# Kernel tuning notes

Measured on AMD Instinct MI355X. Metric: run time of the kernel, lower is better.

Reference implementation:

```python
import jax, jax.numpy as jnp
import numpy as np

C, CB, W, N = 256, 64, 32, 16
F = CB * W  # 2048 lstm features


def setup_inputs() -> dict:
    key = jax.random.key(0)
    ks = jax.random.split(key, 8)
    sc = 1.0 / np.sqrt(F)  # matches torch LSTM uniform(-1/sqrt(H), 1/sqrt(H)) scale
    return {
        "latent": jax.random.normal(ks[0], (N, C, W, W), jnp.float32),
        "w_in": jax.random.normal(ks[1], (CB, C), jnp.float32) * 0.05,
        "b_in": jnp.zeros((CB,), jnp.float32),
        "w_ih0": jax.random.normal(ks[2], (4 * F, F), jnp.float32) * sc,
        "w_hh0": jax.random.normal(ks[3], (4 * F, F), jnp.float32) * sc,
        "b_ih0": jnp.zeros((4 * F,), jnp.float32),
        "b_hh0": jnp.zeros((4 * F,), jnp.float32),
        "w_ih1": jax.random.normal(ks[4], (4 * F, F), jnp.float32) * sc,
        "w_hh1": jax.random.normal(ks[5], (4 * F, F), jnp.float32) * sc,
        "b_ih1": jnp.zeros((4 * F,), jnp.float32),
        "b_hh1": jnp.zeros((4 * F,), jnp.float32),
        "w_out": jax.random.normal(ks[6], (C, CB), jnp.float32) * 0.05,
        "b_out": jnp.zeros((C,), jnp.float32),
    }


def _lstm_cell(xt, h, c, w_ih, w_hh, b):
    # torch gate order: i, f, g, o
    g = xt @ w_ih.T + h @ w_hh.T + b
    i, f, gg, o = jnp.split(g, 4, axis=-1)
    c = jax.nn.sigmoid(f) * c + jax.nn.sigmoid(i) * jnp.tanh(gg)
    h = jax.nn.sigmoid(o) * jnp.tanh(c)
    return h, c


def reference(latent, w_in, b_in, w_ih0, w_hh0, b_ih0, b_hh0,
              w_ih1, w_hh1, b_ih1, b_hh1, w_out, b_out):
    n, ch, w, hgt = latent.shape
    # bottleneck_in: 1x1 conv (Normalizer.NONE / Activation.NONE -> identity)
    x = jnp.einsum('nchw,oc->nohw', latent, w_in) + b_in[None, :, None, None]  # (N,CB,W,H)
    # (N,CB,W,H) -> (N,W,H,CB) -> (N,W,H*CB) -> (W,N,F)
    seq = x.transpose(0, 2, 3, 1).reshape(n, w, -1).transpose(1, 0, 2)

    b0 = b_ih0 + b_hh0
    b1 = b_ih1 + b_hh1

    def step2(carry, xt):
        h0, c0, h1, c1 = carry
        h0, c0 = _lstm_cell(xt, h0, c0, w_ih0, w_hh0, b0)
        h1, c1 = _lstm_cell(h0, h1, c1, w_ih1, w_hh1, b1)
        return (h0, c0, h1, c1), h1

    z = jnp.zeros((n, seq.shape[-1]), latent.dtype)
    state, outs = jax.lax.scan(step2, (z, z, z, z), seq)
    last = outs[-1]  # out[-1] of full-sequence pass

    def ar_step(carry, _):
        st, xt = carry
        st, y = step2(st, xt)
        return (st, y), y

    _, ar_outs = jax.lax.scan(ar_step, (state, last), None, length=w - 1)
    seq_out = jnp.concatenate([last[None], ar_outs], axis=0)  # (W,N,F)

    # (W,N,F) -> (N,W,F) -> (N,W,H,CB) -> (N,CB,W,H)
    gen = seq_out.transpose(1, 0, 2).reshape(n, w, hgt, -1).transpose(0, 3, 1, 2)
    gen = jnp.einsum('nchw,oc->nohw', gen, w_out) + b_out[None, :, None, None]
    # stitch along spatial W axis (dim=2)
    return jnp.concatenate([latent, gen], axis=2)
```

## Files before the change

### kernel.cpp

```cpp
#include <hip/hip_runtime.h>
#include <hip/hip_bf16.h>

#define NB   16
#define FDIM 2048
#define GDIM 8192
#define WSEQ 32
#define CDIM 256
#define CBD  64
#define HGT  32

#define AGENTSC __HIP_MEMORY_SCOPE_AGENT

typedef float f32x4 __attribute__((ext_vector_type(4)));
typedef long  l64x2 __attribute__((ext_vector_type(2)));
typedef _Float16 f16x4 __attribute__((ext_vector_type(4)));
typedef unsigned char u8;

__device__ __forceinline__ float sigf(float x) { return 1.f / (1.f + __expf(-x)); }

__device__ __forceinline__ u8 f32_to_fp8(float f) {
    int w = __builtin_amdgcn_cvt_pk_fp8_f32(f, f, 0, 0);
    return (u8)(w & 0xff);
}

__global__ __launch_bounds__(256) void pack_w(
        const float* __restrict__ wih0, const float* __restrict__ whh0,
        const float* __restrict__ wih1, const float* __restrict__ whh1,
        u8* __restrict__ W0, u8* __restrict__ W1) {
    __shared__ u8 FW[16][4112];
    int b = blockIdx.x;
    int mat = b >> 9, tile = b & 511;
    const float* wih = mat ? wih1 : wih0;
    const float* whh = mat ? whh1 : whh0;
    int p = tile & 1, jt = tile >> 1;
    int tid = threadIdx.x;
    for (int it = 0; it < 32; it += 4) {
        float4 f[4][2];
#pragma unroll
        for (int r = 0; r < 4; ++r) {
            int c = (it + r) & 15, srcsel = (it + r) >> 4;
            int gate = p * 2 + (c >> 3);
            int rr = gate * FDIM + jt * 8 + (c & 7);
            const float* s = (srcsel ? whh : wih) + (size_t)rr * FDIM + tid * 8;
            f[r][0] = *(const float4*)(s);
            f[r][1] = *(const float4*)(s + 4);
        }
#pragma unroll
        for (int r = 0; r < 4; ++r) {
            int c = (it + r) & 15, srcsel = (it + r) >> 4;
            int w0 = __builtin_amdgcn_cvt_pk_fp8_f32(f[r][0].x, f[r][0].y, 0, 0);
            w0     = __builtin_amdgcn_cvt_pk_fp8_f32(f[r][0].z, f[r][0].w, w0, 1);
            int w1 = __builtin_amdgcn_cvt_pk_fp8_f32(f[r][1].x, f[r][1].y, 0, 0);
            w1     = __builtin_amdgcn_cvt_pk_fp8_f32(f[r][1].z, f[r][1].w, w1, 1);
            *(int2*)&FW[c][srcsel * 2048 + tid * 8] = make_int2(w0, w1);
        }
    }
    __syncthreads();
    u8* base = (mat ? W1 : W0) + (size_t)tile * 65536;
#pragma unroll
    for (int w = 0; w < 16; ++w) {
        int q = w * 256 + tid;
        int kc2 = q >> 6, lane = q & 63;
        int c = lane & 15, kg = lane >> 4;
        l64x2 v;
        v.x = *(const long*)&FW[c][kc2 * 64 + kg * 8];
        v.y = *(const long*)&FW[c][kc2 * 64 + 32 + kg * 8];
        *(l64x2*)(base + (size_t)q * 16) = v;
    }
}

__global__ void bias_k(const float* __restrict__ bih0, const float* __restrict__ bhh0,
                       const float* __restrict__ bih1, const float* __restrict__ bhh1,
                       float* __restrict__ b0, float* __restrict__ b1) {
    int i = blockIdx.x * blockDim.x + threadIdx.x;
    if (i < GDIM)            b0[i] = bih0[i] + bhh0[i];
    else if (i < 2 * GDIM) { int j = i - GDIM; b1[j] = bih1[j] + bhh1[j]; }
}

__global__ __launch_bounds__(256) void conv_in(const float* __restrict__ latent,
                        const float* __restrict__ w_in, const float* __restrict__ b_in,
                        u8* __restrict__ seqbP) {
    __shared__ float lat[CDIM * HGT];
    __shared__ float hv[FDIM];
    int b = blockIdx.x; int n = b >> 5; int t = b & 31;
    int tid = threadIdx.x;
    for (int i = 0; i < 32; ++i) {
        int flat = i * 256 + tid;
        int c = flat >> 5, h = flat & 31;
        lat[flat] = latent[(((size_t)n * CDIM + c) * WSEQ + t) * HGT + h];
    }
    __syncthreads();
    int cb = tid & 63;
    int hb = tid >> 6;
    float acc[8];
#pragma unroll
    for (int k = 0; k < 8; ++k) acc[k] = b_in[cb];
    for (int c = 0; c < CDIM; ++c) {
        float wv = w_in[cb * CDIM + c];
#pragma unroll
        for (int k = 0; k < 8; ++k) acc[k] += lat[c * HGT + (hb + k * 4)] * wv;
    }
#pragma unroll
    for (int k = 0; k < 8; ++k) hv[k * 256 + tid] = acc[k];
    __syncthreads();
    union { u8 by[8]; long l; } pk;
#pragma unroll
    for (int i = 0; i < 8; ++i) pk.by[i] = f32_to_fp8(hv[tid * 8 + i]);
    *(long*)(seqbP + (size_t)t * 32768 + (tid >> 2) * 512 + (tid & 3) * 128 + n * 8) = pk.l;
}

__device__ __forceinline__ void load8_plain(const u8* p, long* f) {
    asm volatile("global_load_dwordx2 %0, %1, off"             : "=v"(f[0]) : "v"(p));
    asm volatile("global_load_dwordx2 %0, %1, off offset:512"  : "=v"(f[1]) : "v"(p));
    asm volatile("global_load_dwordx2 %0, %1, off offset:1024" : "=v"(f[2]) : "v"(p));
    asm volatile("global_load_dwordx2 %0, %1, off offset:1536" : "=v"(f[3]) : "v"(p));
    asm volatile("global_load_dwordx2 %0, %1, off offset:2048" : "=v"(f[4]) : "v"(p));
    asm volatile("global_load_dwordx2 %0, %1, off offset:2560" : "=v"(f[5]) : "v"(p));
    asm volatile("global_load_dwordx2 %0, %1, off offset:3072" : "=v"(f[6]) : "v"(p));
    asm volatile("global_load_dwordx2 %0, %1, off offset:3584" : "=v"(f[7]) : "v"(p));
}

__device__ __forceinline__ void vm_wait0() {
    asm volatile("s_waitcnt vmcnt(0)" ::: "memory");
    __builtin_amdgcn_sched_barrier(0);
}

__device__ __forceinline__ void sync_lds() {
    asm volatile("s_waitcnt lgkmcnt(0)" ::: "memory");
    __builtin_amdgcn_s_barrier();
    asm volatile("" ::: "memory");
}

__device__ __forceinline__ f32x4 mfma8(long a, long b, f32x4 acc) {
    return __builtin_amdgcn_mfma_f32_16x16x32_fp8_fp8(a, b, acc, 0, 0, 0);
}

__device__ __forceinline__ void mma8_reg(const long* f, const l64x2* b, f32x4& acc) {
#pragma unroll
    for (int i = 0; i < 4; ++i) {
        acc = mfma8(f[2 * i],     b[i].x, acc);
        acc = mfma8(f[2 * i + 1], b[i].y, acc);
    }
}
__device__ __forceinline__ void mma8_lds(const long* f, const l64x2* bb, f32x4& acc) {
#pragma unroll
    for (int i = 0; i < 4; ++i) {
        l64x2 bl = bb[(size_t)i * 64];
        acc = mfma8(f[2 * i],     bl.x, acc);
        acc = mfma8(f[2 * i + 1], bl.y, acc);
    }
}

__device__ __forceinline__ void store_frag(_Float16* part16, int t, int w,
                                           int kg, int la, f32x4 acc) {
    f16x4 h;
#pragma unroll
    for (int q = 0; q < 4; ++q) h[q] = (_Float16)acc[q];
    *(f16x4*)&part16[(((t * 16 + w) * 16) + la) * 20 + kg * 4] = h;
}

__device__ __forceinline__ void cell_tail16(const _Float16* part16, int jt, int tid,
        float bi, float bf, float bg, float bo, float& cr,
        u8* oA, u8* oB, float* seqSlot) {
    if (tid < 128) {
        int m = tid >> 3, jj = tid & 7;
        float gi = 0.f, gf = 0.f, gg = 0.f, go = 0.f;
#pragma unroll
        for (int w2 = 0; w2 < 16; ++w2) {
            int i0 = (w2 * 16 + jj) * 20 + m;
            gi += (float)part16[i0];
            gf += (float)part16[i0 + 160];
            gg += (float)part16[i0 + 5120];
            go += (float)part16[i0 + 5280];
        }
        float cn = sigf(gf + bf) * cr + sigf(gi + bi) * tanhf(gg + bg);
        float h  = sigf(go + bo) * tanhf(cn);
        cr = cn;
        u8 hb = f32_to_fp8(h);
        int pos = (jt >> 2) * 512 + (jt & 3) * 128 + tid;
        __hip_atomic_store(oA + pos, hb, __ATOMIC_RELAXED, AGENTSC);
        __hip_atomic_store(oB + pos, hb, __ATOMIC_RELAXED, AGENTSC);
        if (seqSlot)
            __hip_atomic_store(seqSlot + m * FDIM + jt * 8 + jj, h,
                               __ATOMIC_RELAXED, AGENTSC);
    }
}

__device__ __forceinline__ void grid_bar(unsigned* slots) {
    __syncthreads();
    if (threadIdx.x < 64) {
        if (threadIdx.x == 0) {
            unsigned one = 1u;
            const unsigned* p = slots + blockIdx.x;
            asm volatile("global_store_dword %0, %1, off sc1"
                         :: "v"(p), "v"(one) : "memory");
        }
        const uint4* q = (const uint4*)slots + threadIdx.x;
        int guard = 0;
        while (++guard < (1 << 22)) {
            uint4 v;
            asm volatile("global_load_dwordx4 %0, %1, off sc1"
                         : "=v"(v) : "v"(q) : "memory");
            asm volatile("s_waitcnt vmcnt(0)" ::: "memory");
            if (__all((v.x & v.y & v.z & v.w) != 0u)) break;
            __builtin_amdgcn_s_sleep(1);
        }
    }
    __syncthreads();
}

__global__ __launch_bounds__(1024, 4) void recurrence(
        const u8* __restrict__ W0, const u8* __restrict__ W1,
        const u8* __restrict__ seqbP,
        const float* __restrict__ b0, const float* __restrict__ b1,
        u8* __restrict__ h0A, u8* __restrict__ h0B,
        u8* __restrict__ h1A, u8* __restrict__ h1B,
        const u8* __restrict__ zb,
        float* __restrict__ sqo, unsigned* __restrict__ arr) {
    __shared__ uint4 w1lds[8192];
    __shared__ _Float16 part16[2 * 16 * 16 * 20];
    const int jt = blockIdx.x, tid = threadIdx.x;
    const int w = tid >> 6, l = tid & 63;
    const int la = l & 15, kg = l >> 4;
    {
        const uint4* src = (const uint4*)(W1 + (size_t)jt * 131072);
        for (int i = tid; i < 8192; i += 1024) w1lds[i] = src[i];
    }
    l64x2 b0pin[8];
#pragma unroll
    for (int t = 0; t < 2; ++t)
#pragma unroll
        for (int i = 0; i < 4; ++i)
            b0pin[t * 4 + i] = *(const l64x2*)(W0 +
                ((size_t)((jt * 2 + t) * 64 + w * 4 + i) * 64 + l) * 16);
    float cr0 = 0.f, cr1 = 0.f;
    float bi0 = 0, bf0 = 0, bg0 = 0, bo0 = 0, bi1 = 0, bf1 = 0, bg1 = 0, bo1 = 0;
    if (tid < 128) {
        int j = jt * 8 + (tid & 7);
        bi0 = b0[j]; bf0 = b0[FDIM + j]; bg0 = b0[2 * FDIM + j]; bo0 = b0[3 * FDIM + j];
        bi1 = b1[j]; bf1 = b1[FDIM + j]; bg1 = b1[2 * FDIM + j]; bo1 = b1[3 * FDIM + j];
    }
    __syncthreads();

    unsigned* bs = arr;
    const l64x2* bbA = (const l64x2*)w1lds + ((size_t)(w * 4) * 64 + l);
    const l64x2* bbB = bbA + (size_t)64 * 64;
    const f32x4 z = {0.f, 0.f, 0.f, 0.f};
    const size_t wl = (size_t)w * 4096 + (size_t)l * 8;
    const size_t wh = (size_t)(w - 8) * 4096 + (size_t)l * 8;
#define HB(arrp, s) ((arrp) + (size_t)(s) * 32768)

    auto l0_phase = [&](const u8* xp, const u8* hp, u8* oA, u8* oB) {
        long f[8];
        load8_plain((w < 8) ? xp + wl : hp + wh, f);
        vm_wait0();
        f32x4 t0 = z, t1 = z;
        mma8_reg(f, b0pin, t0); mma8_reg(f, b0pin + 4, t1);
        store_frag(part16, 0, w, kg, la, t0);
        store_frag(part16, 1, w, kg, la, t1);
        sync_lds();
        cell_tail16(part16, jt, tid, bi0, bf0, bg0, bo0, cr0, oA, oB, nullptr);
    };
    auto l1_phase = [&](const u8* p1, const u8* p2, u8* oA, u8* oB, float* slot) {
        long f[8];
        load8_plain((w < 8) ? p1 + wl : p2 + wh, f);
        vm_wait0();
        f32x4 t0 = z, t1 = z;
        mma8_lds(f, bbA, t0); mma8_lds(f, bbB, t1);
        store_frag(part16, 0, w, kg, la, t0);
        store_frag(part16, 1, w, kg, la, t1);
        sync_lds();
        cell_tail16(part16, jt, tid, bi1, bf1, bg1, bo1, cr1, oA, oB, slot);
    };

    l0_phase(seqbP, zb, HB(h0A, 0), HB(h0B, 0));
    grid_bar(bs); bs += 256;

    for (int s = 0; s <= 30; ++s) {
        long f0[8], f1[8];
        const u8* a0src = (w < 8) ? seqbP + (size_t)(s + 1) * 32768 + wl
                                  : HB(h0A, s) + wh;
        const u8* a1src = (w < 8) ? HB(h0B, s) + wl
                                  : (s == 0 ? zb + wh : HB(h1A, s - 1) + wh);
        load8_plain(a0src, f0);
        load8_plain(a1src, f1);
        vm_wait0();
        f32x4 q00 = z, q01 = z, q10 = z, q11 = z;
        mma8_reg(f0, b0pin, q00); mma8_reg(f0, b0pin + 4, q01);
        mma8_lds(f1, bbA, q10);   mma8_lds(f1, bbB, q11);
        store_frag(part16, 0, w, kg, la, q00);
        store_frag(part16, 1, w, kg, la, q01);
        sync_lds();
        cell_tail16(part16, jt, tid, bi0, bf0, bg0, bo0, cr0,
                    HB(h0A, s + 1), HB(h0B, s + 1), nullptr);
        sync_lds();
        store_frag(part16, 0, w, kg, la, q10);
        store_frag(part16, 1, w, kg, la, q11);
        sync_lds();
        cell_tail16(part16, jt, tid, bi1, bf1, bg1, bo1, cr1,
                    HB(h1A, s), HB(h1B, s), nullptr);
        grid_bar(bs); bs += 256;
    }
    l1_phase(HB(h0B, 31), HB(h1A, 30), HB(h1A, 31), HB(h1B, 31), sqo);
    grid_bar(bs); bs += 256;
    for (int s = 32; s < 63; ++s) {
        l0_phase(HB(h1B, s - 1), HB(h0A, s - 1), HB(h0A, s), HB(h0B, s));
        grid_bar(bs); bs += 256;
        l1_phase(HB(h0B, s), HB(h1A, s - 1), HB(h1A, s), HB(h1B, s),
                 sqo + (size_t)(s - 31) * NB * FDIM);
        if (s != 62) { grid_bar(bs); bs += 256; }
    }
#undef HB
}

__global__ void copy_lat(const float* __restrict__ latent, float* __restrict__ out) {
    size_t i = (size_t)blockIdx.x * blockDim.x + threadIdx.x;
    if (i >= (size_t)1048576) return;
    size_t blk = i >> 8;
    size_t within = i & 255;
    float4 v = ((const float4*)latent)[i];
    ((float4*)out)[blk * 512 + within] = v;
}

__global__ __launch_bounds__(256) void gen_out(const float* __restrict__ seq_out,
                        const float* __restrict__ w_out, const float* __restrict__ b_out,
                        float* __restrict__ out) {
    __shared__ float row[32 * 65];
    int b = blockIdx.x; int n = b >> 5, t = b & 31;
    const float* src = seq_out + ((size_t)t * NB + n) * FDIM;
    for (int i = threadIdx.x; i < FDIM; i += 256)
        row[(i >> 6) * 65 + (i & 63)] = src[i];
    __syncthreads();
    for (int it = 0; it < 32; ++it) {
        int o = it * 256 + threadIdx.x;
        int c = o >> 5, h = o & 31;
        float acc = b_out[c];
#pragma unroll
        for (int cb = 0; cb < CBD; ++cb) acc += row[h * 65 + cb] * w_out[c * CBD + cb];
        out[(((size_t)n * CDIM + c) * 64 + 32 + t) * HGT + h] = acc;
    }
}

extern "C" void kernel_launch(void* const* d_in, const int* in_sizes, int n_in,
                              void* d_out, int out_size, void* d_ws, size_t ws_size,
                              hipStream_t stream) {
    const float* latent = (const float*)d_in[0];
    const float* w_in   = (const float*)d_in[1];
    const float* b_in   = (const float*)d_in[2];
    const float* w_ih0  = (const float*)d_in[3];
    const float* w_hh0  = (const float*)d_in[4];
    const float* b_ih0  = (const float*)d_in[5];
    const float* b_hh0  = (const float*)d_in[6];
    const float* w_ih1  = (const float*)d_in[7];
    const float* w_hh1  = (const float*)d_in[8];
    const float* b_ih1  = (const float*)d_in[9];
    const float* b_hh1  = (const float*)d_in[10];
    const float* w_out  = (const float*)d_in[11];
    const float* b_out  = (const float*)d_in[12];
    float* out = (float*)d_out;
    char* ws = (char*)d_ws;

    size_t off = 0;
    u8*    W0   = (u8*)(ws + off); off += (size_t)512 * 65536;
    u8*    W1   = (u8*)(ws + off); off += (size_t)512 * 65536;
    u8*    seqbP= (u8*)(ws + off); off += (size_t)WSEQ * 32768;
    float* sqo  = (float*)(ws + off); off += (size_t)WSEQ * NB * FDIM * 4;
    u8*    h0A  = (u8*)(ws + off); off += (size_t)64 * 32768;
    u8*    h0B  = (u8*)(ws + off); off += (size_t)64 * 32768;
    u8*    h1A  = (u8*)(ws + off); off += (size_t)64 * 32768;
    u8*    h1B  = (u8*)(ws + off); off += (size_t)64 * 32768;
    char*  zbase = ws + off;
    u8*    zb   = (u8*)(ws + off); off += 32768;
    unsigned* arr = (unsigned*)(ws + off); off += (size_t)94 * 1024;
    size_t zbytes = (size_t)(ws + off - zbase);
    float* b0 = (float*)(ws + off); off += (size_t)GDIM * 4;
    float* b1 = (float*)(ws + off); off += (size_t)GDIM * 4;

    if (ws_size < off) {
        hipMemsetAsync(d_out, 0, (size_t)out_size * 4, stream);
        return;
    }

    hipMemsetAsync(zbase, 0, zbytes, stream);
    pack_w<<<1024, 256, 0, stream>>>(w_ih0, w_hh0, w_ih1, w_hh1, W0, W1);
    bias_k<<<64, 256, 0, stream>>>(b_ih0, b_hh0, b_ih1, b_hh1, b0, b1);
    conv_in<<<512, 256, 0, stream>>>(latent, w_in, b_in, seqbP);
    recurrence<<<256, 1024, 0, stream>>>(W0, W1, seqbP, b0, b1,
                                         h0A, h0B, h1A, h1B, zb, sqo, arr);
    copy_lat<<<4096, 256, 0, stream>>>(latent, out);
    gen_out<<<512, 256, 0, stream>>>(sqo, w_out, b_out, out);
}
```

Before: 767.9 us.

## Pin both layers' weights in registers and run the two cell tails concurrently

Result: slower. 1.083 ms (+41.0%).

```diff
diff --git a/kernel.cpp b/kernel.cpp
--- a/kernel.cpp
+++ b/kernel.cpp
@@ -142,48 +142,37 @@
         acc = mfma8(f[2 * i + 1], b[i].y, acc);
     }
 }
-__device__ __forceinline__ void mma8_lds(const long* f, const l64x2* bb, f32x4& acc) {
-#pragma unroll
-    for (int i = 0; i < 4; ++i) {
-        l64x2 bl = bb[(size_t)i * 64];
-        acc = mfma8(f[2 * i],     bl.x, acc);
-        acc = mfma8(f[2 * i + 1], bl.y, acc);
-    }
-}
-
-__device__ __forceinline__ void store_frag(_Float16* part16, int t, int w,
+
+__device__ __forceinline__ void store_frag(_Float16* P, int t, int w,
                                            int kg, int la, f32x4 acc) {
     f16x4 h;
 #pragma unroll
     for (int q = 0; q < 4; ++q) h[q] = (_Float16)acc[q];
-    *(f16x4*)&part16[(((t * 16 + w) * 16) + la) * 20 + kg * 4] = h;
-}
-
-__device__ __forceinline__ void cell_tail16(const _Float16* part16, int jt, int tid,
+    *(f16x4*)&P[(((t * 16 + w) * 16) + la) * 20 + kg * 4] = h;
+}
+
+__device__ __forceinline__ void cell_tail16(const _Float16* P, int jt, int t2,
         float bi, float bf, float bg, float bo, float& cr,
-        u8* oA, u8* oB, float* seqSlot) {
-    if (tid < 128) {
-        int m = tid >> 3, jj = tid & 7;
-        float gi = 0.f, gf = 0.f, gg = 0.f, go = 0.f;
-#pragma unroll
-        for (int w2 = 0; w2 < 16; ++w2) {
-            int i0 = (w2 * 16 + jj) * 20 + m;
-            gi += (float)part16[i0];
-            gf += (float)part16[i0 + 160];
-            gg += (float)part16[i0 + 5120];
-            go += (float)part16[i0 + 5280];
-        }
-        float cn = sigf(gf + bf) * cr + sigf(gi + bi) * tanhf(gg + bg);
-        float h  = sigf(go + bo) * tanhf(cn);
-        cr = cn;
-        u8 hb = f32_to_fp8(h);
-        int pos = (jt >> 2) * 512 + (jt & 3) * 128 + tid;
-        __hip_atomic_store(oA + pos, hb, __ATOMIC_RELAXED, AGENTSC);
-        __hip_atomic_store(oB + pos, hb, __ATOMIC_RELAXED, AGENTSC);
-        if (seqSlot)
-            __hip_atomic_store(seqSlot + m * FDIM + jt * 8 + jj, h,
-                               __ATOMIC_RELAXED, AGENTSC);
-    }
+        u8* hOut, float* seqSlot) {
+    int m = t2 >> 3, jj = t2 & 7;
+    float gi = 0.f, gf = 0.f, gg = 0.f, go = 0.f;
+#pragma unroll
+    for (int w2 = 0; w2 < 16; ++w2) {
+        int i0 = (w2 * 16 + jj) * 20 + m;
+        gi += (float)P[i0];
+        gf += (float)P[i0 + 160];
+        gg += (float)P[i0 + 5120];
+        go += (float)P[i0 + 5280];
+    }
+    float cn = sigf(gf + bf) * cr + sigf(gi + bi) * tanhf(gg + bg);
+    float h  = sigf(go + bo) * tanhf(cn);
+    cr = cn;
+    u8 hb = f32_to_fp8(h);
+    int pos = (jt >> 2) * 512 + (jt & 3) * 128 + t2;
+    __hip_atomic_store(hOut + pos, hb, __ATOMIC_RELAXED, AGENTSC);
+    if (seqSlot)
+        __hip_atomic_store(seqSlot + m * FDIM + jt * 8 + jj, h,
+                           __ATOMIC_RELAXED, AGENTSC);
 }
 
 __device__ __forceinline__ void grid_bar(unsigned* slots) {
@@ -213,104 +202,122 @@
         const u8* __restrict__ W0, const u8* __restrict__ W1,
         const u8* __restrict__ seqbP,
         const float* __restrict__ b0, const float* __restrict__ b1,
-        u8* __restrict__ h0A, u8* __restrict__ h0B,
-        u8* __restrict__ h1A, u8* __restrict__ h1B,
+        u8* __restrict__ h0buf, u8* __restrict__ h1buf,
         const u8* __restrict__ zb,
         float* __restrict__ sqo, unsigned* __restrict__ arr) {
-    __shared__ uint4 w1lds[8192];
-    __shared__ _Float16 part16[2 * 16 * 16 * 20];
+    __shared__ _Float16 pA[2 * 16 * 16 * 20];
+    __shared__ _Float16 pB[2 * 16 * 16 * 20];
+    __shared__ u8 ldspad[49152];
     const int jt = blockIdx.x, tid = threadIdx.x;
     const int w = tid >> 6, l = tid & 63;
     const int la = l & 15, kg = l >> 4;
-    {
-        const uint4* src = (const uint4*)(W1 + (size_t)jt * 131072);
-        for (int i = tid; i < 8192; i += 1024) w1lds[i] = src[i];
-    }
-    l64x2 b0pin[8];
+    if (tid == 1023) { volatile u8* vp = ldspad; vp[0] = 1; }
+    l64x2 w0pin[8], w1pin[8];
 #pragma unroll
     for (int t = 0; t < 2; ++t)
 #pragma unroll
-        for (int i = 0; i < 4; ++i)
-            b0pin[t * 4 + i] = *(const l64x2*)(W0 +
-                ((size_t)((jt * 2 + t) * 64 + w * 4 + i) * 64 + l) * 16);
-    float cr0 = 0.f, cr1 = 0.f;
-    float bi0 = 0, bf0 = 0, bg0 = 0, bo0 = 0, bi1 = 0, bf1 = 0, bg1 = 0, bo1 = 0;
+        for (int i = 0; i < 4; ++i) {
+            size_t idx = ((size_t)((jt * 2 + t) * 64 + w * 4 + i) * 64 + l) * 16;
+            w0pin[t * 4 + i] = *(const l64x2*)(W0 + idx);
+            w1pin[t * 4 + i] = *(const l64x2*)(W1 + idx);
+        }
+    float cr = 0.f;
+    float bi = 0, bf = 0, bg = 0, bo = 0;
     if (tid < 128) {
         int j = jt * 8 + (tid & 7);
-        bi0 = b0[j]; bf0 = b0[FDIM + j]; bg0 = b0[2 * FDIM + j]; bo0 = b0[3 * FDIM + j];
-        bi1 = b1[j]; bf1 = b1[FDIM + j]; bg1 = b1[2 * FDIM + j]; bo1 = b1[3 * FDIM + j];
+        bi = b0[j]; bf = b0[FDIM + j]; bg = b0[2 * FDIM + j]; bo = b0[3 * FDIM + j];
+    } else if (tid < 256) {
+        int j = jt * 8 + (tid & 7);
+        bi = b1[j]; bf = b1[FDIM + j]; bg = b1[2 * FDIM + j]; bo = b1[3 * FDIM + j];
     }
     __syncthreads();
 
     unsigned* bs = arr;
-    const l64x2* bbA = (const l64x2*)w1lds + ((size_t)(w * 4) * 64 + l);
-    const l64x2* bbB = bbA + (size_t)64 * 64;
     const f32x4 z = {0.f, 0.f, 0.f, 0.f};
     const size_t wl = (size_t)w * 4096 + (size_t)l * 8;
     const size_t wh = (size_t)(w - 8) * 4096 + (size_t)l * 8;
-#define HB(arrp, s) ((arrp) + (size_t)(s) * 32768)
-
-    auto l0_phase = [&](const u8* xp, const u8* hp, u8* oA, u8* oB) {
-        long f[8];
-        load8_plain((w < 8) ? xp + wl : hp + wh, f);
+#define H0(s) (h0buf + (size_t)(s) * 32768)
+#define H1(s) (h1buf + (size_t)(s) * 32768)
+
+    long f0[8], f1[8];
+
+    {
+        load8_plain((w < 8) ? seqbP + wl : zb + wh, f0);
         vm_wait0();
         f32x4 t0 = z, t1 = z;
-        mma8_reg(f, b0pin, t0); mma8_reg(f, b0pin + 4, t1);
-        store_frag(part16, 0, w, kg, la, t0);
-        store_frag(part16, 1, w, kg, la, t1);
+        mma8_reg(f0, w0pin, t0); mma8_reg(f0, w0pin + 4, t1);
+        store_frag(pA, 0, w, kg, la, t0);
+        store_frag(pA, 1, w, kg, la, t1);
         sync_lds();
-        cell_tail16(part16, jt, tid, bi0, bf0, bg0, bo0, cr0, oA, oB, nullptr);
-    };
-    auto l1_phase = [&](const u8* p1, const u8* p2, u8* oA, u8* oB, float* slot) {
-        long f[8];
-        load8_plain((w < 8) ? p1 + wl : p2 + wh, f);
+        if (tid < 128)
+            cell_tail16(pA, jt, tid, bi, bf, bg, bo, cr, H0(0), nullptr);
+    }
+    for (int s = 0; s <= 30; ++s) {
+        if (w < 8) load8_plain(seqbP + (size_t)(s + 1) * 32768 + wl, f0);
+        grid_bar(bs); bs += 256;
+        if (w >= 8) {
+            load8_plain(H0(s) + wh, f0);
+            load8_plain((s ? H1(s - 1) : zb) + wh, f1);
+        } else {
+            load8_plain(H0(s) + wl, f1);
+        }
+        vm_wait0();
+        f32x4 q00 = z, q01 = z, q10 = z, q11 = z;
+        mma8_reg(f0, w0pin, q00); mma8_reg(f0, w0pin + 4, q01);
+        mma8_reg(f1, w1pin, q10); mma8_reg(f1, w1pin + 4, q11);
+        store_frag(pA, 0, w, kg, la, q00);
+        store_frag(pA, 1, w, kg, la, q01);
+        store_frag(pB, 0, w, kg, la, q10);
+        store_frag(pB, 1, w, kg, la, q11);
+        sync_lds();
+        if (tid < 128)
+            cell_tail16(pA, jt, tid, bi, bf, bg, bo, cr, H0(s + 1), nullptr);
+        else if (tid < 256)
+            cell_tail16(pB, jt, tid - 128, bi, bf, bg, bo, cr, H1(s), nullptr);
+    }
+    {
+        grid_bar(bs); bs += 256;
+        load8_plain((w < 8) ? H0(31) + wl : H1(30) + wh, f1);
         vm_wait0();
         f32x4 t0 = z, t1 = z;
-        mma8_lds(f, bbA, t0); mma8_lds(f, bbB, t1);
-        store_frag(part16, 0, w, kg, la, t0);
-        store_frag(part16, 1, w, kg, la, t1);
+        mma8_reg(f1, w1pin, t0); mma8_reg(f1, w1pin + 4, t1);
+        store_frag(pB, 0, w, kg, la, t0);
+        store_frag(pB, 1, w, kg, la, t1);
         sync_lds();
-        cell_tail16(part16, jt, tid, bi1, bf1, bg1, bo1, cr1, oA, oB, slot);
-    };
-
-    l0_phase(seqbP, zb, HB(h0A, 0), HB(h0B, 0));
-    grid_bar(bs); bs += 256;
-
-    for (int s = 0; s <= 30; ++s) {
-        long f0[8], f1[8];
-        const u8* a0src = (w < 8) ? seqbP + (size_t)(s + 1) * 32768 + wl
-                                  : HB(h0A, s) + wh;
-        const u8* a1src = (w < 8) ? HB(h0B, s) + wl
-                                  : (s == 0 ? zb + wh : HB(h1A, s - 1) + wh);
-        load8_plain(a0src, f0);
-        load8_plain(a1src, f1);
-        vm_wait0();
-        f32x4 q00 = z, q01 = z, q10 = z, q11 = z;
-        mma8_reg(f0, b0pin, q00); mma8_reg(f0, b0pin + 4, q01);
-        mma8_lds(f1, bbA, q10);   mma8_lds(f1, bbB, q11);
-        store_frag(part16, 0, w, kg, la, q00);
-        store_frag(part16, 1, w, kg, la, q01);
-        sync_lds();
-        cell_tail16(part16, jt, tid, bi0, bf0, bg0, bo0, cr0,
-                    HB(h0A, s + 1), HB(h0B, s + 1), nullptr);
-        sync_lds();
-        store_frag(part16, 0, w, kg, la, q10);
-        store_frag(part16, 1, w, kg, la, q11);
-        sync_lds();
-        cell_tail16(part16, jt, tid, bi1, bf1, bg1, bo1, cr1,
-                    HB(h1A, s), HB(h1B, s), nullptr);
+        if (tid >= 128 && tid < 256)
+            cell_tail16(pB, jt, tid - 128, bi, bf, bg, bo, cr, H1(31), sqo);
+    }
+    for (int s = 32; s < 63; ++s) {
+        if (w >= 8) load8_plain(H0(s - 1) + wh, f0);
         grid_bar(bs); bs += 256;
-    }
-    l1_phase(HB(h0B, 31), HB(h1A, 30), HB(h1A, 31), HB(h1B, 31), sqo);
-    grid_bar(bs); bs += 256;
-    for (int s = 32; s < 63; ++s) {
-        l0_phase(HB(h1B, s - 1), HB(h0A, s - 1), HB(h0A, s), HB(h0B, s));
+        if (w < 8) load8_plain(H1(s - 1) + wl, f0);
+        vm_wait0();
+        {
+            f32x4 t0 = z, t1 = z;
+            mma8_reg(f0, w0pin, t0); mma8_reg(f0, w0pin + 4, t1);
+            store_frag(pA, 0, w, kg, la, t0);
+            store_frag(pA, 1, w, kg, la, t1);
+            sync_lds();
+            if (tid < 128)
+                cell_tail16(pA, jt, tid, bi, bf, bg, bo, cr, H0(s), nullptr);
+        }
+        if (w >= 8) load8_plain(H1(s - 1) + wh, f1);
         grid_bar(bs); bs += 256;
-        l1_phase(HB(h0B, s), HB(h1A, s - 1), HB(h1A, s), HB(h1B, s),
-                 sqo + (size_t)(s - 31) * NB * FDIM);
-        if (s != 62) { grid_bar(bs); bs += 256; }
-    }
-#undef HB
+        if (w < 8) load8_plain(H0(s) + wl, f1);
+        vm_wait0();
+        {
+            f32x4 t0 = z, t1 = z;
+            mma8_reg(f1, w1pin, t0); mma8_reg(f1, w1pin + 4, t1);
+            store_frag(pB, 0, w, kg, la, t0);
+            store_frag(pB, 1, w, kg, la, t1);
+            sync_lds();
+            if (tid >= 128 && tid < 256)
+                cell_tail16(pB, jt, tid - 128, bi, bf, bg, bo, cr, H1(s),
+                            sqo + (size_t)(s - 31) * NB * FDIM);
+        }
+    }
+#undef H0
+#undef H1
 }
 
 __global__ void copy_lat(const float* __restrict__ latent, float* __restrict__ out) {
@@ -365,10 +372,8 @@
     u8*    W1   = (u8*)(ws + off); off += (size_t)512 * 65536;
     u8*    seqbP= (u8*)(ws + off); off += (size_t)WSEQ * 32768;
     float* sqo  = (float*)(ws + off); off += (size_t)WSEQ * NB * FDIM * 4;
-    u8*    h0A  = (u8*)(ws + off); off += (size_t)64 * 32768;
-    u8*    h0B  = (u8*)(ws + off); off += (size_t)64 * 32768;
-    u8*    h1A  = (u8*)(ws + off); off += (size_t)64 * 32768;
-    u8*    h1B  = (u8*)(ws + off); off += (size_t)64 * 32768;
+    u8*    h0buf= (u8*)(ws + off); off += (size_t)64 * 32768;
+    u8*    h1buf= (u8*)(ws + off); off += (size_t)64 * 32768;
     char*  zbase = ws + off;
     u8*    zb   = (u8*)(ws + off); off += 32768;
     unsigned* arr = (unsigned*)(ws + off); off += (size_t)94 * 1024;
@@ -386,7 +391,7 @@
     bias_k<<<64, 256, 0, stream>>>(b_ih0, b_hh0, b_ih1, b_hh1, b0, b1);
     conv_in<<<512, 256, 0, stream>>>(latent, w_in, b_in, seqbP);
     recurrence<<<256, 1024, 0, stream>>>(W0, W1, seqbP, b0, b1,
-                                         h0A, h0B, h1A, h1B, zb, sqo, arr);
+                                         h0buf, h1buf, zb, sqo, arr);
     copy_lat<<<4096, 256, 0, stream>>>(latent, out);
     gen_out<<<512, 256, 0, stream>>>(sqo, w_out, b_out, out);
 }
```
